# Performance work log

Hardware: AMD Instinct MI355X
Metric: run time of the kernel (lower is better)

Reference implementation:

```python
import jax, jax.numpy as jnp
import numpy as np

BN_EPS = 1e-5


def setup_inputs() -> dict:
    key = jax.random.key(0)
    k1, k2 = jax.random.split(key)
    B, IN, OUT = 8192, 4096, 4096
    x = jax.random.normal(k1, (B, IN), dtype=jnp.float32)
    weight = jax.random.normal(k2, (OUT, IN), dtype=jnp.float32) * 0.1
    bias = jnp.zeros((OUT,), dtype=jnp.float32)
    return {"x": x, "weight": weight, "bias": bias}


def reference(x, weight, bias):
    # Binarize activations and weights to {-1, 0, +1} via sign (sign(0)=0, matching torch).
    bx = jnp.sign(x)            # [B, IN]
    bw = jnp.sign(weight)       # [OUT, IN]
    out = jnp.einsum('bi,oi->bo', bx, bw) + bias  # F.linear
    # BatchNorm1d, training mode, affine=False: normalize with batch mean / biased var.
    mean = jnp.mean(out, axis=0)
    var = jnp.mean(jnp.square(out - mean), axis=0)
    return (out - mean) * jax.lax.rsqrt(var + BN_EPS)
```

## Files before the change

kernel.cpp:

```cpp
#include <hip/hip_runtime.h>
#include <stdint.h>

#define B_ROWS 8192
#define IN_DIM 4096
#define OUT_DIM 4096
#define BN_EPS 1e-5f

#define BM 256
#define BLKN 256
#define BKB 128
#define NKT (IN_DIM / BKB)
#define NIT (NKT / 2)

typedef __attribute__((ext_vector_type(4))) int i32x4;

__device__ __forceinline__ int sign_byte(float f) {
    int s = (f > 0.f) ? 1 : ((f < 0.f) ? -1 : 0);
    return s & 0xFF;
}

__global__ void pack_i8(const float* __restrict__ in, int* __restrict__ out) {
    int gid = blockIdx.x * blockDim.x + threadIdx.x;
    float4 v = reinterpret_cast<const float4*>(in)[gid];
    out[gid] = sign_byte(v.x) | (sign_byte(v.y) << 8) |
               (sign_byte(v.z) << 16) | (sign_byte(v.w) << 24);
}

__device__ __forceinline__ void stage_pair(const int8_t* g0, int8_t* l0) {
    __builtin_amdgcn_global_load_lds(
        (const __attribute__((address_space(1))) void*)g0,
        (__attribute__((address_space(3))) void*)l0, 16, 0, 0);
    __builtin_amdgcn_global_load_lds(
        (const __attribute__((address_space(1))) void*)(g0 + (size_t)128 * IN_DIM),
        (__attribute__((address_space(3))) void*)(l0 + 128 * BKB), 16, 0, 0);
}

template <int FB>
__device__ __forceinline__ void load_frag4(i32x4 d[4][2], const int8_t* base,
                                           int off0, int off1) {
#pragma unroll
    for (int f = 0; f < 4; ++f) {
        d[f][0] = *reinterpret_cast<const i32x4*>(base + (FB + f) * (16 * BKB) + off0);
        d[f][1] = *reinterpret_cast<const i32x4*>(base + (FB + f) * (16 * BKB) + off1);
    }
}

template <int FB>
__device__ __forceinline__ void load_frag2(i32x4 d[2][2], const int8_t* base,
                                           int off0, int off1) {
#pragma unroll
    for (int f = 0; f < 2; ++f) {
        d[f][0] = *reinterpret_cast<const i32x4*>(base + (FB + f) * (16 * BKB) + off0);
        d[f][1] = *reinterpret_cast<const i32x4*>(base + (FB + f) * (16 * BKB) + off1);
    }
}

template <int AM, int AN>
__device__ __forceinline__ void mfma_quad(i32x4 acc[8][4], const i32x4 a[4][2],
                                          const i32x4 b[2][2]) {
#pragma unroll
    for (int mf = 0; mf < 4; ++mf)
#pragma unroll
        for (int nf = 0; nf < 2; ++nf) {
            acc[AM + mf][AN + nf] = __builtin_amdgcn_mfma_i32_16x16x64_i8(
                a[mf][0], b[nf][0], acc[AM + mf][AN + nf], 0, 0, 0);
            acc[AM + mf][AN + nf] = __builtin_amdgcn_mfma_i32_16x16x64_i8(
                a[mf][1], b[nf][1], acc[AM + mf][AN + nf], 0, 0, 0);
        }
}

#define PHASE_MID()                                             \
    __builtin_amdgcn_s_barrier();                               \
    asm volatile("s_waitcnt lgkmcnt(0)" ::: "memory");          \
    __builtin_amdgcn_sched_barrier(0);                          \
    __builtin_amdgcn_s_setprio(1)

#define PHASE_END()                                             \
    __builtin_amdgcn_s_setprio(0);                              \
    __builtin_amdgcn_s_barrier()

#define PHASE_END_VM()                                          \
    __builtin_amdgcn_s_setprio(0);                              \
    asm volatile("s_waitcnt vmcnt(6)" ::: "memory");            \
    __builtin_amdgcn_s_barrier()

__global__ __launch_bounds__(512, 2) void bin_gemm_i8(
    const int8_t* __restrict__ A,
    const int8_t* __restrict__ W,
    float* __restrict__ out,
    float* __restrict__ colsum,
    float* __restrict__ colsumsq)
{
    __shared__ __align__(16) int8_t lds[2][2][BM * BKB];
    __shared__ float s_sum[BLKN];
    __shared__ float s_sq[BLKN];

    const int t      = threadIdx.x;
    const int lane   = t & 63;
    const int wave   = t >> 6;
    const int wm     = wave >> 2;
    const int wn     = wave & 3;
    const int lane16 = lane & 15;
    const int quad   = lane >> 4;

    const int flat = blockIdx.y * gridDim.x + blockIdx.x;
    const int swz  = (flat & 7) * (512 / 8) + (flat >> 3);
    const int row0 = (swz >> 4) * BM;
    const int col0 = (swz & 15) * BLKN;

    if (t < BLKN) { s_sum[t] = 0.f; s_sq[t] = 0.f; }

    const int r6 = t >> 3;
    const int c8 = t & 7;
    const int gslot = ((c8 ^ (r6 & 7)) << 4);
    const int rA0 = r6;
    const int rB0 = r6 + (r6 & 32);

    const int8_t* pA = A + (size_t)(row0 + rA0) * IN_DIM + gslot;
    const int8_t* pW = W + (size_t)(col0 + rB0) * IN_DIM + gslot;
    int8_t* lA0 = &lds[0][0][rA0 * BKB + c8 * 16];
    int8_t* lB0 = &lds[0][1][rB0 * BKB + c8 * 16];

    const int sw   = lane & 7;
    const int off0 = ((quad ^ sw) << 4);
    const int off1 = (((4 + quad) ^ sw) << 4);
    const int8_t* rA = &lds[0][0][(wm * 128 + lane16) * BKB];
    const int8_t* rB = &lds[0][1][(wn * 64 + lane16) * BKB];

    i32x4 acc[8][4] = {};
    i32x4 alo[4][2], ahi[4][2], bb[2][2];

    stage_pair(pA,                             lA0);
    stage_pair(pA + (size_t)64 * IN_DIM,       lA0 + 64 * BKB);
    stage_pair(pW,                             lB0);
    stage_pair(pW + (size_t)32 * IN_DIM,       lB0 + 32 * BKB);
    stage_pair(pA + BKB,                       lA0 + 65536);
    stage_pair(pA + (size_t)64 * IN_DIM + BKB, lA0 + 65536 + 64 * BKB);
    stage_pair(pW + BKB,                       lB0 + 65536);
    asm volatile("s_waitcnt vmcnt(6)" ::: "memory");
    __builtin_amdgcn_s_barrier();

#pragma unroll 1
    for (int it = 0; it < NIT; ++it) {
        const int tc1 = (2 * it + 1) & (NKT - 1);
        const int tn0 = (2 * it + 2) & (NKT - 1);
        const int tn1 = (2 * it + 3) & (NKT - 1);

        load_frag4<0>(alo, rA, off0, off1);
        load_frag2<0>(bb, rB, off0, off1);
        stage_pair(pW + (size_t)32 * IN_DIM + tc1 * BKB, lB0 + 65536 + 32 * BKB);
        PHASE_MID();
        mfma_quad<0, 0>(acc, alo, bb);
        PHASE_END();

        load_frag4<4>(ahi, rA, off0, off1);
        stage_pair(pA + tn0 * BKB, lA0);
        PHASE_MID();
        mfma_quad<4, 0>(acc, ahi, bb);
        PHASE_END();

        load_frag2<2>(bb, rB, off0, off1);
        stage_pair(pA + (size_t)64 * IN_DIM + tn0 * BKB, lA0 + 64 * BKB);
        PHASE_MID();
        mfma_quad<4, 2>(acc, ahi, bb);
        PHASE_END();

        stage_pair(pW + tn0 * BKB, lB0);
        PHASE_MID();
        mfma_quad<0, 2>(acc, alo, bb);
        PHASE_END_VM();

        load_frag4<0>(alo, rA + 65536, off0, off1);
        load_frag2<0>(bb, rB + 65536, off0, off1);
        stage_pair(pW + (size_t)32 * IN_DIM + tn0 * BKB, lB0 + 32 * BKB);
        PHASE_MID();
        mfma_quad<0, 0>(acc, alo, bb);
        PHASE_END();

        load_frag4<4>(ahi, rA + 65536, off0, off1);
        stage_pair(pA + tn1 * BKB, lA0 + 65536);
        PHASE_MID();
        mfma_quad<4, 0>(acc, ahi, bb);
        PHASE_END();

        load_frag2<2>(bb, rB + 65536, off0, off1);
        stage_pair(pA + (size_t)64 * IN_DIM + tn1 * BKB, lA0 + 65536 + 64 * BKB);
        PHASE_MID();
        mfma_quad<4, 2>(acc, ahi, bb);
        PHASE_END();

        stage_pair(pW + tn1 * BKB, lB0 + 65536);
        PHASE_MID();
        mfma_quad<0, 2>(acc, alo, bb);
        PHASE_END_VM();
    }

    float csum[4] = {0.f, 0.f, 0.f, 0.f};
    float csq[4]  = {0.f, 0.f, 0.f, 0.f};
#pragma unroll
    for (int mf = 0; mf < 8; ++mf) {
#pragma unroll
        for (int r = 0; r < 4; ++r) {
            int grow = row0 + wm * 128 + mf * 16 + quad * 4 + r;
            float* orow = out + (size_t)grow * OUT_DIM + col0 + wn * 64 + lane16;
#pragma unroll
            for (int nf = 0; nf < 4; ++nf) {
                float v = (float)acc[mf][nf][r];
                orow[nf * 16] = v;
                csum[nf] += v;
                csq[nf]  += v * v;
            }
        }
    }
#pragma unroll
    for (int nf = 0; nf < 4; ++nf) {
        csum[nf] += __shfl_xor(csum[nf], 16);
        csum[nf] += __shfl_xor(csum[nf], 32);
        csq[nf]  += __shfl_xor(csq[nf], 16);
        csq[nf]  += __shfl_xor(csq[nf], 32);
    }
    if (quad == 0) {
#pragma unroll
        for (int nf = 0; nf < 4; ++nf) {
            atomicAdd(&s_sum[wn * 64 + nf * 16 + lane16], csum[nf]);
            atomicAdd(&s_sq [wn * 64 + nf * 16 + lane16], csq[nf]);
        }
    }
    __syncthreads();
    if (t < BLKN) {
        atomicAdd(&colsum[col0 + t],   s_sum[t]);
        atomicAdd(&colsumsq[col0 + t], s_sq[t]);
    }
}

__global__ void bn_stats(const float* __restrict__ colsum,
                         const float* __restrict__ colsumsq,
                         float* __restrict__ mean, float* __restrict__ rstd) {
    int o = blockIdx.x * blockDim.x + threadIdx.x;
    float m = colsum[o] * (1.0f / B_ROWS);
    float v = colsumsq[o] * (1.0f / B_ROWS) - m * m;
    mean[o] = m;
    rstd[o] = rsqrtf(v + BN_EPS);
}

__global__ void bn_apply(float* __restrict__ out,
                         const float* __restrict__ mean,
                         const float* __restrict__ rstd) {
    size_t f = (size_t)blockIdx.x * blockDim.x + threadIdx.x;
    int c4 = (int)(f & (OUT_DIM / 4 - 1));
    float4 v = reinterpret_cast<float4*>(out)[f];
    float4 m = reinterpret_cast<const float4*>(mean)[c4];
    float4 r = reinterpret_cast<const float4*>(rstd)[c4];
    v.x = (v.x - m.x) * r.x;
    v.y = (v.y - m.y) * r.y;
    v.z = (v.z - m.z) * r.z;
    v.w = (v.w - m.w) * r.w;
    reinterpret_cast<float4*>(out)[f] = v;
}

extern "C" void kernel_launch(void* const* d_in, const int* in_sizes, int n_in,
                              void* d_out, int out_size, void* d_ws, size_t ws_size,
                              hipStream_t stream) {
    const float* x = (const float*)d_in[0];
    const float* w = (const float*)d_in[1];
    float* out = (float*)d_out;

    uint8_t* ws = (uint8_t*)d_ws;
    int8_t* xb = (int8_t*)ws;
    int8_t* wb = (int8_t*)(ws + (size_t)B_ROWS * IN_DIM);
    float* colsum   = (float*)(ws + (size_t)B_ROWS * IN_DIM
                                  + (size_t)OUT_DIM * IN_DIM);
    float* colsumsq = colsum + OUT_DIM;
    float* mean     = colsumsq + OUT_DIM;
    float* rstd     = mean + OUT_DIM;

    hipMemsetAsync(colsum, 0, 2 * OUT_DIM * sizeof(float), stream);

    pack_i8<<<(B_ROWS * IN_DIM / 4) / 256, 256, 0, stream>>>(x, (int*)xb);
    pack_i8<<<(OUT_DIM * IN_DIM / 4) / 256, 256, 0, stream>>>(w, (int*)wb);

    bin_gemm_i8<<<dim3(OUT_DIM / BLKN, B_ROWS / BM), 512, 0, stream>>>(
        xb, wb, out, colsum, colsumsq);

    bn_stats<<<OUT_DIM / 256, 256, 0, stream>>>(colsum, colsumsq, mean, rstd);

    bn_apply<<<(unsigned)((size_t)B_ROWS * OUT_DIM / 4 / 256), 256, 0, stream>>>(
        out, mean, rstd);
}
```

Baseline: 437.0 us.

## Prefetch LDS fragments a phase ahead and merge the two pack kernels

Reworks the GEMM main loop schedule so each phase's LDS fragment reads are issued one phase before the MFMAs that consume them. This removes the explicit lgkmcnt(0) wait before each MFMA block and uses separate bb01/bb23 B-fragment registers. It also reorders MFMA issue by k-slice, changes the prologue staging and vmcnt waits, and fuses the two sign-packing kernels into one launch. The cost is higher register pressure, and the looser LDS read/write ordering against the async global-to-LDS copies risks races if the waits are mis-set.

```diff
diff --git a/kernel.cpp b/kernel.cpp
--- a/kernel.cpp
+++ b/kernel.cpp
@@ -19,10 +19,16 @@
     return s & 0xFF;
 }
 
-__global__ void pack_i8(const float* __restrict__ in, int* __restrict__ out) {
+#define XN (B_ROWS * IN_DIM / 4)
+
+__global__ void pack_both(const float* __restrict__ x, const float* __restrict__ w,
+                          int* __restrict__ xb, int* __restrict__ wb) {
     int gid = blockIdx.x * blockDim.x + threadIdx.x;
-    float4 v = reinterpret_cast<const float4*>(in)[gid];
-    out[gid] = sign_byte(v.x) | (sign_byte(v.y) << 8) |
+    const float* src = (gid < XN) ? x : w;
+    int*         dst = (gid < XN) ? xb : wb;
+    int          idx = (gid < XN) ? gid : gid - XN;
+    float4 v = reinterpret_cast<const float4*>(src)[idx];
+    dst[idx] = sign_byte(v.x) | (sign_byte(v.y) << 8) |
                (sign_byte(v.z) << 16) | (sign_byte(v.w) << 24);
 }
 
@@ -59,30 +65,31 @@
 __device__ __forceinline__ void mfma_quad(i32x4 acc[8][4], const i32x4 a[4][2],
                                           const i32x4 b[2][2]) {
 #pragma unroll
-    for (int mf = 0; mf < 4; ++mf)
-#pragma unroll
-        for (int nf = 0; nf < 2; ++nf) {
-            acc[AM + mf][AN + nf] = __builtin_amdgcn_mfma_i32_16x16x64_i8(
-                a[mf][0], b[nf][0], acc[AM + mf][AN + nf], 0, 0, 0);
-            acc[AM + mf][AN + nf] = __builtin_amdgcn_mfma_i32_16x16x64_i8(
-                a[mf][1], b[nf][1], acc[AM + mf][AN + nf], 0, 0, 0);
-        }
-}
-
-#define PHASE_MID()                                             \
+    for (int ks = 0; ks < 2; ++ks)
+#pragma unroll
+        for (int mf = 0; mf < 4; ++mf)
+#pragma unroll
+            for (int nf = 0; nf < 2; ++nf)
+                acc[AM + mf][AN + nf] = __builtin_amdgcn_mfma_i32_16x16x64_i8(
+                    a[mf][ks], b[nf][ks], acc[AM + mf][AN + nf], 0, 0, 0);
+}
+
+#define WIN_END()                                               \
+    __builtin_amdgcn_sched_barrier(0);                          \
     __builtin_amdgcn_s_barrier();                               \
-    asm volatile("s_waitcnt lgkmcnt(0)" ::: "memory");          \
     __builtin_amdgcn_sched_barrier(0);                          \
     __builtin_amdgcn_s_setprio(1)
 
-#define PHASE_END()                                             \
+#define MFMA_END()                                              \
     __builtin_amdgcn_s_setprio(0);                              \
-    __builtin_amdgcn_s_barrier()
-
-#define PHASE_END_VM()                                          \
+    __builtin_amdgcn_s_barrier();                               \
+    __builtin_amdgcn_sched_barrier(0)
+
+#define MFMA_END_VM(N)                                          \
     __builtin_amdgcn_s_setprio(0);                              \
-    asm volatile("s_waitcnt vmcnt(6)" ::: "memory");            \
-    __builtin_amdgcn_s_barrier()
+    asm volatile("s_waitcnt vmcnt(" #N ")" ::: "memory");       \
+    __builtin_amdgcn_s_barrier();                               \
+    __builtin_amdgcn_sched_barrier(0)
 
 __global__ __launch_bounds__(512, 2) void bin_gemm_i8(
     const int8_t* __restrict__ A,
@@ -128,17 +135,19 @@
     const int8_t* rB = &lds[0][1][(wn * 64 + lane16) * BKB];
 
     i32x4 acc[8][4] = {};
-    i32x4 alo[4][2], ahi[4][2], bb[2][2];
-
-    stage_pair(pA,                             lA0);
-    stage_pair(pA + (size_t)64 * IN_DIM,       lA0 + 64 * BKB);
-    stage_pair(pW,                             lB0);
-    stage_pair(pW + (size_t)32 * IN_DIM,       lB0 + 32 * BKB);
-    stage_pair(pA + BKB,                       lA0 + 65536);
-    stage_pair(pA + (size_t)64 * IN_DIM + BKB, lA0 + 65536 + 64 * BKB);
-    stage_pair(pW + BKB,                       lB0 + 65536);
-    asm volatile("s_waitcnt vmcnt(6)" ::: "memory");
+    i32x4 alo[4][2], ahi[4][2], bb01[2][2], bb23[2][2];
+
+    stage_pair(pA,                       lA0);
+    stage_pair(pA + (size_t)64 * IN_DIM, lA0 + 64 * BKB);
+    stage_pair(pW,                       lB0);
+    stage_pair(pW + (size_t)32 * IN_DIM, lB0 + 32 * BKB);
+    stage_pair(pA + BKB,                 lA0 + 65536);
+    stage_pair(pW + BKB,                 lB0 + 65536);
+    asm volatile("s_waitcnt vmcnt(0)" ::: "memory");
     __builtin_amdgcn_s_barrier();
+    __builtin_amdgcn_sched_barrier(0);
+    load_frag4<0>(alo,  rA, off0, off1);
+    load_frag2<0>(bb01, rB, off0, off1);
 
 #pragma unroll 1
     for (int it = 0; it < NIT; ++it) {
@@ -146,53 +155,53 @@
         const int tn0 = (2 * it + 2) & (NKT - 1);
         const int tn1 = (2 * it + 3) & (NKT - 1);
 
-        load_frag4<0>(alo, rA, off0, off1);
-        load_frag2<0>(bb, rB, off0, off1);
+        load_frag2<2>(bb23, rB, off0, off1);
+        stage_pair(pA + (size_t)64 * IN_DIM + tc1 * BKB, lA0 + 65536 + 64 * BKB);
+        WIN_END();
+        mfma_quad<0, 0>(acc, alo, bb01);
+        MFMA_END();
+
+        load_frag4<4>(ahi, rA, off0, off1);
         stage_pair(pW + (size_t)32 * IN_DIM + tc1 * BKB, lB0 + 65536 + 32 * BKB);
-        PHASE_MID();
-        mfma_quad<0, 0>(acc, alo, bb);
-        PHASE_END();
-
-        load_frag4<4>(ahi, rA, off0, off1);
+        WIN_END();
+        mfma_quad<0, 2>(acc, alo, bb23);
+        MFMA_END();
+
         stage_pair(pA + tn0 * BKB, lA0);
-        PHASE_MID();
-        mfma_quad<4, 0>(acc, ahi, bb);
-        PHASE_END();
-
-        load_frag2<2>(bb, rB, off0, off1);
+        WIN_END();
+        mfma_quad<4, 0>(acc, ahi, bb01);
+        MFMA_END_VM(6);
+
+        load_frag4<0>(alo,  rA + 65536, off0, off1);
+        load_frag2<0>(bb01, rB + 65536, off0, off1);
+        stage_pair(pW + tn0 * BKB, lB0);
+        WIN_END();
+        mfma_quad<4, 2>(acc, ahi, bb23);
+        MFMA_END_VM(4);
+
+        load_frag2<2>(bb23, rB + 65536, off0, off1);
         stage_pair(pA + (size_t)64 * IN_DIM + tn0 * BKB, lA0 + 64 * BKB);
-        PHASE_MID();
-        mfma_quad<4, 2>(acc, ahi, bb);
-        PHASE_END();
-
-        stage_pair(pW + tn0 * BKB, lB0);
-        PHASE_MID();
-        mfma_quad<0, 2>(acc, alo, bb);
-        PHASE_END_VM();
-
-        load_frag4<0>(alo, rA + 65536, off0, off1);
-        load_frag2<0>(bb, rB + 65536, off0, off1);
+        WIN_END();
+        mfma_quad<0, 0>(acc, alo, bb01);
+        MFMA_END();
+
+        load_frag4<4>(ahi, rA + 65536, off0, off1);
         stage_pair(pW + (size_t)32 * IN_DIM + tn0 * BKB, lB0 + 32 * BKB);
-        PHASE_MID();
-        mfma_quad<0, 0>(acc, alo, bb);
-        PHASE_END();
-
-        load_frag4<4>(ahi, rA + 65536, off0, off1);
+        WIN_END();
+        mfma_quad<0, 2>(acc, alo, bb23);
+        MFMA_END();
+
         stage_pair(pA + tn1 * BKB, lA0 + 65536);
-        PHASE_MID();
-        mfma_quad<4, 0>(acc, ahi, bb);
-        PHASE_END();
-
-        load_frag2<2>(bb, rB + 65536, off0, off1);
-        stage_pair(pA + (size_t)64 * IN_DIM + tn1 * BKB, lA0 + 65536 + 64 * BKB);
-        PHASE_MID();
-        mfma_quad<4, 2>(acc, ahi, bb);
-        PHASE_END();
-
+        WIN_END();
+        mfma_quad<4, 0>(acc, ahi, bb01);
+        MFMA_END_VM(6);
+
+        load_frag4<0>(alo,  rA, off0, off1);
+        load_frag2<0>(bb01, rB, off0, off1);
         stage_pair(pW + tn1 * BKB, lB0 + 65536);
-        PHASE_MID();
-        mfma_quad<0, 2>(acc, alo, bb);
-        PHASE_END_VM();
+        WIN_END();
+        mfma_quad<4, 2>(acc, ahi, bb23);
+        MFMA_END_VM(4);
     }
 
     float csum[4] = {0.f, 0.f, 0.f, 0.f};
@@ -276,8 +285,8 @@
 
     hipMemsetAsync(colsum, 0, 2 * OUT_DIM * sizeof(float), stream);
 
-    pack_i8<<<(B_ROWS * IN_DIM / 4) / 256, 256, 0, stream>>>(x, (int*)xb);
-    pack_i8<<<(OUT_DIM * IN_DIM / 4) / 256, 256, 0, stream>>>(w, (int*)wb);
+    pack_both<<<((B_ROWS + OUT_DIM) * (IN_DIM / 4)) / 256, 256, 0, stream>>>(
+        x, w, (int*)xb, (int*)wb);
 
     bin_gemm_i8<<<dim3(OUT_DIM / BLKN, B_ROWS / BM), 512, 0, stream>>>(
         xb, wb, out, colsum, colsumsq);
```

Result: slower. 512.2 us (+17.2%).
